# Kernel optimization log

Measured on AMD Instinct MI355X. Metric: run time of the kernel, lower is better.

The kernel has to match this reference:

```python
import jax, jax.numpy as jnp
import numpy as np

N, E, IN_DIM, OUT_DIM = 12288, 6144, 256, 256


def setup_inputs() -> dict:
    key = jax.random.key(0)
    k1, k2, k3, k4, k5 = jax.random.split(key, 5)
    x = jax.random.normal(k1, (N, IN_DIM), dtype=jnp.float32)
    # incidence-like matrix (dense, values in [0,1))
    H = jax.random.uniform(k2, (N, E), dtype=jnp.float32)
    # degree-normalizer diagonals: positive entries on the diagonal
    dv = jax.random.uniform(k3, (N,), dtype=jnp.float32, minval=0.1, maxval=1.0)
    de = jax.random.uniform(k4, (E,), dtype=jnp.float32, minval=0.1, maxval=1.0)
    D_v_neg_sqrt = jnp.diag(dv)
    D_e_neg = jnp.diag(de)
    # Linear params (xavier-like weight, zero bias)
    W = jax.random.normal(k5, (IN_DIM, OUT_DIM), dtype=jnp.float32) * (1.0 / np.sqrt(IN_DIM))
    b = jnp.zeros((OUT_DIM,), dtype=jnp.float32)
    return {"x": x, "H": H, "D_v_neg_sqrt": D_v_neg_sqrt, "D_e_neg": D_e_neg, "W": W, "b": b}


def reference(x, H, D_v_neg_sqrt, D_e_neg, W, b):
    # x_transformed = Linear(x)
    x_t = x @ W + b                      # [N, out]
    x_norm = D_v_neg_sqrt @ x_t          # [N, out]
    x_he = H.T @ x_norm                  # [E, out]
    x_he_norm = D_e_neg @ x_he           # [E, out]
    x_node = H @ x_he_norm               # [N, out]
    out = D_v_neg_sqrt @ x_node          # [N, out]
    # dropout is identity in eval mode
    return out
```

## Files before the change

kernel.cpp:

```cpp
#include <hip/hip_runtime.h>

#define NN 12288
#define NE 6144
#define ND 256

typedef __attribute__((ext_vector_type(8))) short short8;
typedef __attribute__((ext_vector_type(4))) float f32x4;
typedef unsigned short u16;
typedef unsigned int u32;

__device__ inline u16 f2bf(float f) {
  union { float f; u32 u; } v; v.f = f;
  u32 r = v.u + 0x7fffu + ((v.u >> 16) & 1u);
  return (u16)(r >> 16);
}

__device__ inline void gll16(const void* g, void* l) {
  __builtin_amdgcn_global_load_lds(
      (const __attribute__((address_space(1))) u32*)g,
      (__attribute__((address_space(3))) u32*)l, 16, 0, 0);
}

__device__ inline void stage_B(const u16* __restrict__ Bg, int ldb, int k0,
                               u16* __restrict__ Blds) {
  const int w = threadIdx.x >> 6;
  const int lane = threadIdx.x & 63;
  const int dd = lane >> 2, p = lane & 3;
#pragma unroll
  for (int s = 0; s < 4; ++s) {
    const int dbase = (w * 4 + s) * 16;
    const int n = dbase + dd;
    const int c = (p - (n >> 1)) & 3;
    gll16(Bg + (size_t)n * ldb + k0 + c * 8, Blds + dbase * 32);
  }
}

__device__ inline short8 load_B(const u16* __restrict__ Blds, int n, int quad) {
  const int p = (quad + (n >> 1)) & 3;
  return *(const short8*)(Blds + n * 32 + p * 8);
}

__global__ __launch_bounds__(256) void k_xform(
    const float* __restrict__ x, const u16* __restrict__ Wt,
    const float* __restrict__ b, const float* __restrict__ dv,
    u16* __restrict__ xnt) {
  __shared__ u16 Alds[64 * 40];
  __shared__ u16 Blds[256 * 32];
  const int tid = threadIdx.x;
  const int w = tid >> 6, lane = tid & 63, ln = lane & 15, quad = lane >> 4;
  const int m0 = blockIdx.x * 64;
  const int am = tid >> 2, ac = (tid & 3) * 8;
  f32x4 acc[4][4] = {};
  for (int kt = 0; kt < ND / 32; ++kt) {
    const int k0 = kt * 32;
    __syncthreads();
    stage_B(Wt, ND, k0, Blds);
    const float4* pa = (const float4*)(x + (size_t)(m0 + am) * ND + k0 + ac);
    float4 f0 = pa[0], f1 = pa[1];
    short8 av;
    av[0] = (short)f2bf(f0.x); av[1] = (short)f2bf(f0.y);
    av[2] = (short)f2bf(f0.z); av[3] = (short)f2bf(f0.w);
    av[4] = (short)f2bf(f1.x); av[5] = (short)f2bf(f1.y);
    av[6] = (short)f2bf(f1.z); av[7] = (short)f2bf(f1.w);
    *(short8*)(Alds + am * 40 + ac) = av;
    __syncthreads();
    short8 af[4];
#pragma unroll
    for (int mt = 0; mt < 4; ++mt)
      af[mt] = *(const short8*)(Alds + (mt * 16 + ln) * 40 + quad * 8);
#pragma unroll
    for (int nt = 0; nt < 4; ++nt) {
      short8 bf = load_B(Blds, w * 64 + nt * 16 + ln, quad);
#pragma unroll
      for (int mt = 0; mt < 4; ++mt)
        acc[nt][mt] = __builtin_amdgcn_mfma_f32_16x16x32_bf16(af[mt], bf, acc[nt][mt], 0, 0, 0);
    }
  }
#pragma unroll
  for (int nt = 0; nt < 4; ++nt) {
    const int d = w * 64 + nt * 16 + ln;
    const float bb = b[d];
#pragma unroll
    for (int mt = 0; mt < 4; ++mt) {
      const int vb = m0 + mt * 16 + quad * 4;
      f32x4 a = acc[nt][mt];
      union { u16 h[4]; uint2 u; } pk;
#pragma unroll
      for (int r = 0; r < 4; ++r) pk.h[r] = f2bf(dv[vb + r] * (a[r] + bb));
      *(uint2*)(xnt + (size_t)d * NN + vb) = pk.u;
    }
  }
}

__global__ __launch_bounds__(256) void k_gemm1s(
    const float* __restrict__ H, const u16* __restrict__ xnt,
    float* __restrict__ P1) {
  __shared__ u16 Alds[64 * 40];
  __shared__ u16 Blds[256 * 32];
  const int tid = threadIdx.x;
  const int w = tid >> 6, lane = tid & 63, ln = lane & 15, quad = lane >> 4;
  const int e0 = blockIdx.x * 64;
  const int kbase = blockIdx.y * 1536;
  const int p2 = tid & 3, ea = tid >> 2;
  f32x4 acc[4][4] = {};
  for (int kt = 0; kt < 48; ++kt) {
    const int k0 = kbase + kt * 32;
    __syncthreads();
    stage_B(xnt, NN, k0, Blds);
#pragma unroll
    for (int i = 0; i < 4; ++i) {
      const int p = p2 + i * 4;
      const int v = k0 + p * 2;
      float g0 = H[(size_t)v * NE + e0 + ea];
      float g1 = H[(size_t)(v + 1) * NE + e0 + ea];
      u32 pk = (u32)f2bf(g0) | ((u32)f2bf(g1) << 16);
      *(u32*)(Alds + ea * 40 + p * 2) = pk;
    }
    __syncthreads();
    short8 af[4];
#pragma unroll
    for (int mt = 0; mt < 4; ++mt)
      af[mt] = *(const short8*)(Alds + (mt * 16 + ln) * 40 + quad * 8);
#pragma unroll
    for (int nt = 0; nt < 4; ++nt) {
      short8 bf = load_B(Blds, w * 64 + nt * 16 + ln, quad);
#pragma unroll
      for (int mt = 0; mt < 4; ++mt)
        acc[nt][mt] = __builtin_amdgcn_mfma_f32_16x16x32_bf16(af[mt], bf, acc[nt][mt], 0, 0, 0);
    }
  }
  float* P = P1 + (size_t)blockIdx.y * NE * ND;
#pragma unroll
  for (int nt = 0; nt < 4; ++nt) {
    const int d = w * 64 + nt * 16 + ln;
#pragma unroll
    for (int mt = 0; mt < 4; ++mt) {
      const int eb = e0 + mt * 16 + quad * 4;
      f32x4 a = acc[nt][mt];
#pragma unroll
      for (int r = 0; r < 4; ++r)
        P[(size_t)(eb + r) * ND + d] = a[r];
    }
  }
}

__global__ __launch_bounds__(256) void k_red1(
    const float* __restrict__ P1, const float* __restrict__ de,
    u16* __restrict__ xhet) {
  const int tid = threadIdx.x;
  const int e0 = blockIdx.x * 16;
  union { u16 h[16]; uint4 q[2]; } pk;
#pragma unroll
  for (int i = 0; i < 16; ++i) {
    float s = 0.f;
#pragma unroll
    for (int c = 0; c < 8; ++c)
      s += P1[(size_t)c * NE * ND + (size_t)(e0 + i) * ND + tid];
    pk.h[i] = f2bf(de[e0 + i] * s);
  }
  uint4* dst = (uint4*)(xhet + (size_t)tid * NE + e0);
  dst[0] = pk.q[0];
  dst[1] = pk.q[1];
}

__global__ __launch_bounds__(256) void k_gemm2s(
    const float* __restrict__ H, const u16* __restrict__ xhet,
    float* __restrict__ P2) {
  __shared__ u16 Alds[64 * 40];
  __shared__ u16 Blds[256 * 32];
  const int tid = threadIdx.x;
  const int w = tid >> 6, lane = tid & 63, ln = lane & 15, quad = lane >> 4;
  const int m0 = blockIdx.x * 64;
  const int kbase = blockIdx.y * 1536;
  const int am = tid >> 2, ac = (tid & 3) * 8;
  f32x4 acc[4][4] = {};
  for (int kt = 0; kt < 48; ++kt) {
    const int k0 = kbase + kt * 32;
    __syncthreads();
    stage_B(xhet, NE, k0, Blds);
    const float4* pa = (const float4*)(H + (size_t)(m0 + am) * NE + k0 + ac);
    float4 f0 = pa[0], f1 = pa[1];
    short8 av;
    av[0] = (short)f2bf(f0.x); av[1] = (short)f2bf(f0.y);
    av[2] = (short)f2bf(f0.z); av[3] = (short)f2bf(f0.w);
    av[4] = (short)f2bf(f1.x); av[5] = (short)f2bf(f1.y);
    av[6] = (short)f2bf(f1.z); av[7] = (short)f2bf(f1.w);
    *(short8*)(Alds + am * 40 + ac) = av;
    __syncthreads();
    short8 af[4];
#pragma unroll
    for (int mt = 0; mt < 4; ++mt)
      af[mt] = *(const short8*)(Alds + (mt * 16 + ln) * 40 + quad * 8);
#pragma unroll
    for (int nt = 0; nt < 4; ++nt) {
      short8 bf = load_B(Blds, w * 64 + nt * 16 + ln, quad);
#pragma unroll
      for (int mt = 0; mt < 4; ++mt)
        acc[nt][mt] = __builtin_amdgcn_mfma_f32_16x16x32_bf16(af[mt], bf, acc[nt][mt], 0, 0, 0);
    }
  }
  float* P = P2 + (size_t)blockIdx.y * NN * ND;
#pragma unroll
  for (int nt = 0; nt < 4; ++nt) {
    const int d = w * 64 + nt * 16 + ln;
#pragma unroll
    for (int mt = 0; mt < 4; ++mt) {
      const int vb = m0 + mt * 16 + quad * 4;
      f32x4 a = acc[nt][mt];
#pragma unroll
      for (int r = 0; r < 4; ++r)
        P[(size_t)(vb + r) * ND + d] = a[r];
    }
  }
}

__global__ __launch_bounds__(256) void k_red2(
    const float* __restrict__ P2, const float* __restrict__ dv,
    float* __restrict__ out) {
  const int tid = threadIdx.x;
  const int v0 = blockIdx.x * 16;
#pragma unroll
  for (int i = 0; i < 16; ++i) {
    float s = 0.f;
#pragma unroll
    for (int c = 0; c < 4; ++c)
      s += P2[(size_t)c * NN * ND + (size_t)(v0 + i) * ND + tid];
    out[(size_t)(v0 + i) * ND + tid] = dv[v0 + i] * s;
  }
}

__global__ __launch_bounds__(256) void k_prep(
    const float* __restrict__ W, const float* __restrict__ Dv,
    const float* __restrict__ De, u16* __restrict__ Wt,
    float* __restrict__ dv, float* __restrict__ de) {
  const int t = blockIdx.x * 256 + threadIdx.x;
  const int d = t >> 8, k = t & 255;
  Wt[d * 256 + k] = f2bf(W[k * 256 + d]);
  if (t < NN) dv[t] = Dv[(size_t)t * (NN + 1)];
  if (t < NE) de[t] = De[(size_t)t * (NE + 1)];
}

extern "C" void kernel_launch(void* const* d_in, const int* in_sizes, int n_in,
                              void* d_out, int out_size, void* d_ws, size_t ws_size,
                              hipStream_t stream) {
  const float* x  = (const float*)d_in[0];
  const float* H  = (const float*)d_in[1];
  const float* Dv = (const float*)d_in[2];
  const float* De = (const float*)d_in[3];
  const float* W  = (const float*)d_in[4];
  const float* b  = (const float*)d_in[5];
  float* out = (float*)d_out;
  char* ws = (char*)d_ws;
  u16* xnt   = (u16*)ws;
  u16* xhet  = (u16*)(ws + 6291456);
  u16* Wt    = (u16*)(ws + 9437184);
  float* dv  = (float*)(ws + 9568256);
  float* de  = (float*)(ws + 9617408);
  float* P1  = (float*)(ws + 9641984);
  float* P2  = (float*)(ws + 59973632);

  hipLaunchKernelGGL(k_prep,   dim3(256), dim3(256), 0, stream, W, Dv, De, Wt, dv, de);
  hipLaunchKernelGGL(k_xform,  dim3(NN / 64), dim3(256), 0, stream, x, Wt, b, dv, xnt);
  hipLaunchKernelGGL(k_gemm1s, dim3(NE / 64, 8), dim3(256), 0, stream, H, xnt, P1);
  hipLaunchKernelGGL(k_red1,   dim3(NE / 16), dim3(256), 0, stream, P1, de, xhet);
  hipLaunchKernelGGL(k_gemm2s, dim3(NN / 64, 4), dim3(256), 0, stream, H, xhet, P2);
  hipLaunchKernelGGL(k_red2,   dim3(NN / 16), dim3(256), 0, stream, P2, dv, out);
}
```

Baseline: 1.081 ms.

## Double-buffer LDS tiles to overlap global loads with MFMA compute

Converts the three GEMM kernels to a two-stage software pipeline. Each now holds two LDS buffers, prefetches the next K-tile of A (into registers) and B (via global_load_lds) while running MFMAs on the current tile, and needs one barrier per iteration instead of two. This is meant to hide global memory latency behind matrix compute. The cost is doubled LDS use per block (about 42KB), which may lower occupancy, and more live registers for the prefetched A values.

```diff
diff --git a/kernel.cpp b/kernel.cpp
--- a/kernel.cpp
+++ b/kernel.cpp
@@ -40,42 +40,61 @@
   return *(const short8*)(Blds + n * 32 + p * 8);
 }
 
+__device__ inline void compute_step(const u16* __restrict__ Al,
+                                    const u16* __restrict__ Bl, int w, int ln,
+                                    int quad, f32x4 (&acc)[4][4]) {
+  short8 af[4];
+#pragma unroll
+  for (int mt = 0; mt < 4; ++mt)
+    af[mt] = *(const short8*)(Al + (mt * 16 + ln) * 40 + quad * 8);
+#pragma unroll
+  for (int nt = 0; nt < 4; ++nt) {
+    short8 bf = load_B(Bl, w * 64 + nt * 16 + ln, quad);
+#pragma unroll
+    for (int mt = 0; mt < 4; ++mt)
+      acc[nt][mt] = __builtin_amdgcn_mfma_f32_16x16x32_bf16(af[mt], bf, acc[nt][mt], 0, 0, 0);
+  }
+}
+
 __global__ __launch_bounds__(256) void k_xform(
     const float* __restrict__ x, const u16* __restrict__ Wt,
     const float* __restrict__ b, const float* __restrict__ dv,
     u16* __restrict__ xnt) {
-  __shared__ u16 Alds[64 * 40];
-  __shared__ u16 Blds[256 * 32];
+  __shared__ u16 Alds[2][64 * 40];
+  __shared__ u16 Blds[2][256 * 32];
   const int tid = threadIdx.x;
   const int w = tid >> 6, lane = tid & 63, ln = lane & 15, quad = lane >> 4;
   const int m0 = blockIdx.x * 64;
   const int am = tid >> 2, ac = (tid & 3) * 8;
   f32x4 acc[4][4] = {};
-  for (int kt = 0; kt < ND / 32; ++kt) {
-    const int k0 = kt * 32;
+  stage_B(Wt, ND, 0, Blds[0]);
+  {
+    const float4* pa = (const float4*)(x + (size_t)(m0 + am) * ND + ac);
+    float4 f0 = pa[0], f1 = pa[1];
+    short8 av;
+    av[0] = (short)f2bf(f0.x); av[1] = (short)f2bf(f0.y);
+    av[2] = (short)f2bf(f0.z); av[3] = (short)f2bf(f0.w);
+    av[4] = (short)f2bf(f1.x); av[5] = (short)f2bf(f1.y);
+    av[6] = (short)f2bf(f1.z); av[7] = (short)f2bf(f1.w);
+    *(short8*)(Alds[0] + am * 40 + ac) = av;
+  }
+  __syncthreads();
+  for (int kt = 0; kt < ND / 32 - 1; ++kt) {
+    const int cur = kt & 1, nxt = cur ^ 1;
+    const int k1 = (kt + 1) * 32;
+    stage_B(Wt, ND, k1, Blds[nxt]);
+    const float4* pa = (const float4*)(x + (size_t)(m0 + am) * ND + k1 + ac);
+    float4 f0 = pa[0], f1 = pa[1];
+    compute_step(Alds[cur], Blds[cur], w, ln, quad, acc);
+    short8 av;
+    av[0] = (short)f2bf(f0.x); av[1] = (short)f2bf(f0.y);
+    av[2] = (short)f2bf(f0.z); av[3] = (short)f2bf(f0.w);
+    av[4] = (short)f2bf(f1.x); av[5] = (short)f2bf(f1.y);
+    av[6] = (short)f2bf(f1.z); av[7] = (short)f2bf(f1.w);
+    *(short8*)(Alds[nxt] + am * 40 + ac) = av;
     __syncthreads();
-    stage_B(Wt, ND, k0, Blds);
-    const float4* pa = (const float4*)(x + (size_t)(m0 + am) * ND + k0 + ac);
-    float4 f0 = pa[0], f1 = pa[1];
-    short8 av;
-    av[0] = (short)f2bf(f0.x); av[1] = (short)f2bf(f0.y);
-    av[2] = (short)f2bf(f0.z); av[3] = (short)f2bf(f0.w);
-    av[4] = (short)f2bf(f1.x); av[5] = (short)f2bf(f1.y);
-    av[6] = (short)f2bf(f1.z); av[7] = (short)f2bf(f1.w);
-    *(short8*)(Alds + am * 40 + ac) = av;
-    __syncthreads();
-    short8 af[4];
-#pragma unroll
-    for (int mt = 0; mt < 4; ++mt)
-      af[mt] = *(const short8*)(Alds + (mt * 16 + ln) * 40 + quad * 8);
-#pragma unroll
-    for (int nt = 0; nt < 4; ++nt) {
-      short8 bf = load_B(Blds, w * 64 + nt * 16 + ln, quad);
-#pragma unroll
-      for (int mt = 0; mt < 4; ++mt)
-        acc[nt][mt] = __builtin_amdgcn_mfma_f32_16x16x32_bf16(af[mt], bf, acc[nt][mt], 0, 0, 0);
-    }
-  }
+  }
+  compute_step(Alds[1], Blds[1], w, ln, quad, acc);
 #pragma unroll
   for (int nt = 0; nt < 4; ++nt) {
     const int d = w * 64 + nt * 16 + ln;
@@ -95,40 +114,49 @@
 __global__ __launch_bounds__(256) void k_gemm1s(
     const float* __restrict__ H, const u16* __restrict__ xnt,
     float* __restrict__ P1) {
-  __shared__ u16 Alds[64 * 40];
-  __shared__ u16 Blds[256 * 32];
+  __shared__ u16 Alds[2][64 * 40];
+  __shared__ u16 Blds[2][256 * 32];
   const int tid = threadIdx.x;
   const int w = tid >> 6, lane = tid & 63, ln = lane & 15, quad = lane >> 4;
   const int e0 = blockIdx.x * 64;
   const int kbase = blockIdx.y * 1536;
   const int p2 = tid & 3, ea = tid >> 2;
   f32x4 acc[4][4] = {};
-  for (int kt = 0; kt < 48; ++kt) {
-    const int k0 = kbase + kt * 32;
-    __syncthreads();
-    stage_B(xnt, NN, k0, Blds);
+  float g[8];
+  stage_B(xnt, NN, kbase, Blds[0]);
+#pragma unroll
+  for (int i = 0; i < 4; ++i) {
+    const int v = kbase + (p2 + i * 4) * 2;
+    g[2 * i] = H[(size_t)v * NE + e0 + ea];
+    g[2 * i + 1] = H[(size_t)(v + 1) * NE + e0 + ea];
+  }
+#pragma unroll
+  for (int i = 0; i < 4; ++i) {
+    const int p = p2 + i * 4;
+    u32 pk = (u32)f2bf(g[2 * i]) | ((u32)f2bf(g[2 * i + 1]) << 16);
+    *(u32*)(Alds[0] + ea * 40 + p * 2) = pk;
+  }
+  __syncthreads();
+  for (int kt = 0; kt < 47; ++kt) {
+    const int cur = kt & 1, nxt = cur ^ 1;
+    const int k1 = kbase + (kt + 1) * 32;
+    stage_B(xnt, NN, k1, Blds[nxt]);
+#pragma unroll
+    for (int i = 0; i < 4; ++i) {
+      const int v = k1 + (p2 + i * 4) * 2;
+      g[2 * i] = H[(size_t)v * NE + e0 + ea];
+      g[2 * i + 1] = H[(size_t)(v + 1) * NE + e0 + ea];
+    }
+    compute_step(Alds[cur], Blds[cur], w, ln, quad, acc);
 #pragma unroll
     for (int i = 0; i < 4; ++i) {
       const int p = p2 + i * 4;
-      const int v = k0 + p * 2;
-      float g0 = H[(size_t)v * NE + e0 + ea];
-      float g1 = H[(size_t)(v + 1) * NE + e0 + ea];
-      u32 pk = (u32)f2bf(g0) | ((u32)f2bf(g1) << 16);
-      *(u32*)(Alds + ea * 40 + p * 2) = pk;
+      u32 pk = (u32)f2bf(g[2 * i]) | ((u32)f2bf(g[2 * i + 1]) << 16);
+      *(u32*)(Alds[nxt] + ea * 40 + p * 2) = pk;
     }
     __syncthreads();
-    short8 af[4];
-#pragma unroll
-    for (int mt = 0; mt < 4; ++mt)
-      af[mt] = *(const short8*)(Alds + (mt * 16 + ln) * 40 + quad * 8);
-#pragma unroll
-    for (int nt = 0; nt < 4; ++nt) {
-      short8 bf = load_B(Blds, w * 64 + nt * 16 + ln, quad);
-#pragma unroll
-      for (int mt = 0; mt < 4; ++mt)
-        acc[nt][mt] = __builtin_amdgcn_mfma_f32_16x16x32_bf16(af[mt], bf, acc[nt][mt], 0, 0, 0);
-    }
-  }
+  }
+  compute_step(Alds[1], Blds[1], w, ln, quad, acc);
   float* P = P1 + (size_t)blockIdx.y * NE * ND;
 #pragma unroll
   for (int nt = 0; nt < 4; ++nt) {
@@ -166,39 +194,42 @@
 __global__ __launch_bounds__(256) void k_gemm2s(
     const float* __restrict__ H, const u16* __restrict__ xhet,
     float* __restrict__ P2) {
-  __shared__ u16 Alds[64 * 40];
-  __shared__ u16 Blds[256 * 32];
+  __shared__ u16 Alds[2][64 * 40];
+  __shared__ u16 Blds[2][256 * 32];
   const int tid = threadIdx.x;
   const int w = tid >> 6, lane = tid & 63, ln = lane & 15, quad = lane >> 4;
   const int m0 = blockIdx.x * 64;
   const int kbase = blockIdx.y * 1536;
   const int am = tid >> 2, ac = (tid & 3) * 8;
   f32x4 acc[4][4] = {};
-  for (int kt = 0; kt < 48; ++kt) {
-    const int k0 = kbase + kt * 32;
+  stage_B(xhet, NE, kbase, Blds[0]);
+  {
+    const float4* pa = (const float4*)(H + (size_t)(m0 + am) * NE + kbase + ac);
+    float4 f0 = pa[0], f1 = pa[1];
+    short8 av;
+    av[0] = (short)f2bf(f0.x); av[1] = (short)f2bf(f0.y);
+    av[2] = (short)f2bf(f0.z); av[3] = (short)f2bf(f0.w);
+    av[4] = (short)f2bf(f1.x); av[5] = (short)f2bf(f1.y);
+    av[6] = (short)f2bf(f1.z); av[7] = (short)f2bf(f1.w);
+    *(short8*)(Alds[0] + am * 40 + ac) = av;
+  }
+  __syncthreads();
+  for (int kt = 0; kt < 47; ++kt) {
+    const int cur = kt & 1, nxt = cur ^ 1;
+    const int k1 = kbase + (kt + 1) * 32;
+    stage_B(xhet, NE, k1, Blds[nxt]);
+    const float4* pa = (const float4*)(H + (size_t)(m0 + am) * NE + k1 + ac);
+    float4 f0 = pa[0], f1 = pa[1];
+    compute_step(Alds[cur], Blds[cur], w, ln, quad, acc);
+    short8 av;
+    av[0] = (short)f2bf(f0.x); av[1] = (short)f2bf(f0.y);
+    av[2] = (short)f2bf(f0.z); av[3] = (short)f2bf(f0.w);
+    av[4] = (short)f2bf(f1.x); av[5] = (short)f2bf(f1.y);
+    av[6] = (short)f2bf(f1.z); av[7] = (short)f2bf(f1.w);
+    *(short8*)(Alds[nxt] + am * 40 + ac) = av;
     __syncthreads();
-    stage_B(xhet, NE, k0, Blds);
-    const float4* pa = (const float4*)(H + (size_t)(m0 + am) * NE + k0 + ac);
-    float4 f0 = pa[0], f1 = pa[1];
-    short8 av;
-    av[0] = (short)f2bf(f0.x); av[1] = (short)f2bf(f0.y);
-    av[2] = (short)f2bf(f0.z); av[3] = (short)f2bf(f0.w);
-    av[4] = (short)f2bf(f1.x); av[5] = (short)f2bf(f1.y);
-    av[6] = (short)f2bf(f1.z); av[7] = (short)f2bf(f1.w);
-    *(short8*)(Alds + am * 40 + ac) = av;
-    __syncthreads();
-    short8 af[4];
-#pragma unroll
-    for (int mt = 0; mt < 4; ++mt)
-      af[mt] = *(const short8*)(Alds + (mt * 16 + ln) * 40 + quad * 8);
-#pragma unroll
-    for (int nt = 0; nt < 4; ++nt) {
-      short8 bf = load_B(Blds, w * 64 + nt * 16 + ln, quad);
-#pragma unroll
-      for (int mt = 0; mt < 4; ++mt)
-        acc[nt][mt] = __builtin_amdgcn_mfma_f32_16x16x32_bf16(af[mt], bf, acc[nt][mt], 0, 0, 0);
-    }
-  }
+  }
+  compute_step(Alds[1], Blds[1], w, ln, quad, acc);
   float* P = P2 + (size_t)blockIdx.y * NN * ND;
 #pragma unroll
   for (int nt = 0; nt < 4; ++nt) {
```

Result: no change. 1.080 ms (-0.1%).

## Fuse all stages into one cooperative persistent kernel with grid syncs

Applied to the files above, without the earlier changes.

Replaces the six separate launches with a single cooperative kernel of 512 blocks (two per CU on 256 CUs) that runs the prep, transform, both split-K GEMMs and both reductions in sequence, separated by grid-wide barriers. Tiles are reshaped to 48-row blocks with larger K splits (4 and 2 chunks) so the fixed grid covers each GEMM exactly in one wave. This removes inter-kernel launch gaps and tail effects. In exchange, the smaller M tiles reduce per-block reuse, the grid barriers add their own cost, and the transform stage uses only 16-row tasks with one wave loading A. The old multi-kernel path stays as a fallback if the cooperative launch fails.

```diff
diff --git a/kernel.cpp b/kernel.cpp
--- a/kernel.cpp
+++ b/kernel.cpp
@@ -1,4 +1,7 @@
 #include <hip/hip_runtime.h>
+#include <hip/hip_cooperative_groups.h>
+
+namespace cg = cooperative_groups;
 
 #define NN 12288
 #define NE 6144
@@ -38,6 +41,195 @@
 __device__ inline short8 load_B(const u16* __restrict__ Blds, int n, int quad) {
   const int p = (quad + (n >> 1)) & 3;
   return *(const short8*)(Blds + n * 32 + p * 8);
+}
+
+template <int MT>
+__device__ inline void compute_tile(const u16* __restrict__ Al,
+                                    const u16* __restrict__ Bl, int w, int ln,
+                                    int quad, f32x4 (&acc)[4][MT]) {
+  short8 af[MT];
+#pragma unroll
+  for (int mt = 0; mt < MT; ++mt)
+    af[mt] = *(const short8*)(Al + (mt * 16 + ln) * 40 + quad * 8);
+#pragma unroll
+  for (int nt = 0; nt < 4; ++nt) {
+    short8 bf = load_B(Bl, w * 64 + nt * 16 + ln, quad);
+#pragma unroll
+    for (int mt = 0; mt < MT; ++mt)
+      acc[nt][mt] = __builtin_amdgcn_mfma_f32_16x16x32_bf16(af[mt], bf, acc[nt][mt], 0, 0, 0);
+  }
+}
+
+__global__ __launch_bounds__(256, 2) void mega(
+    const float* __restrict__ x, const float* __restrict__ H,
+    const float* __restrict__ Dv, const float* __restrict__ De,
+    const float* __restrict__ W, const float* __restrict__ b,
+    float* __restrict__ out, u16* __restrict__ xnt, u16* __restrict__ xhet,
+    u16* __restrict__ Wt, float* __restrict__ dv, float* __restrict__ de,
+    float* __restrict__ P1, float* __restrict__ P2) {
+  cg::grid_group gg = cg::this_grid();
+  __shared__ u16 Alds[64 * 40];
+  __shared__ u16 Blds[256 * 32];
+  const int tid = threadIdx.x;
+  const int bid = blockIdx.x;
+  const int w = tid >> 6, lane = tid & 63, ln = lane & 15, quad = lane >> 4;
+
+  {
+    const int t = bid * 256 + tid;
+    if (t < 65536) {
+      const int d = t >> 8, k = t & 255;
+      Wt[d * 256 + k] = f2bf(W[k * 256 + d]);
+    }
+    if (t < NN) dv[t] = Dv[(size_t)t * (NN + 1)];
+    if (t < NE) de[t] = De[(size_t)t * (NE + 1)];
+  }
+  gg.sync();
+
+  for (int task = bid; task < 768; task += 512) {
+    const int m0 = task * 16;
+    f32x4 acc[4] = {};
+    for (int kt = 0; kt < 8; ++kt) {
+      const int k0 = kt * 32;
+      __syncthreads();
+      stage_B(Wt, ND, k0, Blds);
+      if (tid < 64) {
+        const int am = tid >> 2, ac2 = (tid & 3) * 8;
+        const float4* pa = (const float4*)(x + (size_t)(m0 + am) * ND + k0 + ac2);
+        float4 f0 = pa[0], f1 = pa[1];
+        short8 av;
+        av[0] = (short)f2bf(f0.x); av[1] = (short)f2bf(f0.y);
+        av[2] = (short)f2bf(f0.z); av[3] = (short)f2bf(f0.w);
+        av[4] = (short)f2bf(f1.x); av[5] = (short)f2bf(f1.y);
+        av[6] = (short)f2bf(f1.z); av[7] = (short)f2bf(f1.w);
+        *(short8*)(Alds + am * 40 + ac2) = av;
+      }
+      __syncthreads();
+      short8 af = *(const short8*)(Alds + ln * 40 + quad * 8);
+#pragma unroll
+      for (int nt = 0; nt < 4; ++nt) {
+        short8 bf = load_B(Blds, w * 64 + nt * 16 + ln, quad);
+        acc[nt] = __builtin_amdgcn_mfma_f32_16x16x32_bf16(af, bf, acc[nt], 0, 0, 0);
+      }
+    }
+#pragma unroll
+    for (int nt = 0; nt < 4; ++nt) {
+      const int d = w * 64 + nt * 16 + ln;
+      const float bb = b[d];
+      const int vb = m0 + quad * 4;
+      f32x4 a = acc[nt];
+      union { u16 h[4]; uint2 u; } pk;
+#pragma unroll
+      for (int r = 0; r < 4; ++r) pk.h[r] = f2bf(dv[vb + r] * (a[r] + bb));
+      *(uint2*)(xnt + (size_t)d * NN + vb) = pk.u;
+    }
+  }
+  gg.sync();
+
+  {
+    const int e0 = (bid & 127) * 48;
+    const int kc = bid >> 7;
+    const int kbase = kc * 3072;
+    const int p2 = tid & 3, ea = tid >> 2;
+    f32x4 acc[4][3] = {};
+    for (int kt = 0; kt < 96; ++kt) {
+      const int k0 = kbase + kt * 32;
+      __syncthreads();
+      stage_B(xnt, NN, k0, Blds);
+      if (ea < 48) {
+#pragma unroll
+        for (int i = 0; i < 4; ++i) {
+          const int p = p2 + i * 4;
+          const int v = k0 + p * 2;
+          float g0 = H[(size_t)v * NE + e0 + ea];
+          float g1 = H[(size_t)(v + 1) * NE + e0 + ea];
+          u32 pk = (u32)f2bf(g0) | ((u32)f2bf(g1) << 16);
+          *(u32*)(Alds + ea * 40 + p * 2) = pk;
+        }
+      }
+      __syncthreads();
+      compute_tile<3>(Alds, Blds, w, ln, quad, acc);
+    }
+    float* P = P1 + (size_t)kc * NE * ND;
+#pragma unroll
+    for (int nt = 0; nt < 4; ++nt) {
+      const int d = w * 64 + nt * 16 + ln;
+#pragma unroll
+      for (int mt = 0; mt < 3; ++mt) {
+        const int eb = e0 + mt * 16 + quad * 4;
+        f32x4 a = acc[nt][mt];
+#pragma unroll
+        for (int r = 0; r < 4; ++r)
+          P[(size_t)(eb + r) * ND + d] = a[r];
+      }
+    }
+  }
+  gg.sync();
+
+  if (bid < 384) {
+    const int e0 = bid * 16;
+    union { u16 h[16]; uint4 q[2]; } pk;
+#pragma unroll
+    for (int i = 0; i < 16; ++i) {
+      float s = 0.f;
+#pragma unroll
+      for (int c = 0; c < 4; ++c)
+        s += P1[(size_t)c * NE * ND + (size_t)(e0 + i) * ND + tid];
+      pk.h[i] = f2bf(de[e0 + i] * s);
+    }
+    uint4* dst = (uint4*)(xhet + (size_t)tid * NE + e0);
+    dst[0] = pk.q[0];
+    dst[1] = pk.q[1];
+  }
+  gg.sync();
+
+  {
+    const int m0 = (bid & 255) * 48;
+    const int kc = bid >> 8;
+    const int kbase = kc * 3072;
+    const int am = tid >> 2, ac2 = (tid & 3) * 8;
+    f32x4 acc[4][3] = {};
+    for (int kt = 0; kt < 96; ++kt) {
+      const int k0 = kbase + kt * 32;
+      __syncthreads();
+      stage_B(xhet, NE, k0, Blds);
+      if (am < 48) {
+        const float4* pa = (const float4*)(H + (size_t)(m0 + am) * NE + k0 + ac2);
+        float4 f0 = pa[0], f1 = pa[1];
+        short8 av;
+        av[0] = (short)f2bf(f0.x); av[1] = (short)f2bf(f0.y);
+        av[2] = (short)f2bf(f0.z); av[3] = (short)f2bf(f0.w);
+        av[4] = (short)f2bf(f1.x); av[5] = (short)f2bf(f1.y);
+        av[6] = (short)f2bf(f1.z); av[7] = (short)f2bf(f1.w);
+        *(short8*)(Alds + am * 40 + ac2) = av;
+      }
+      __syncthreads();
+      compute_tile<3>(Alds, Blds, w, ln, quad, acc);
+    }
+    float* P = P2 + (size_t)kc * NN * ND;
+#pragma unroll
+    for (int nt = 0; nt < 4; ++nt) {
+      const int d = w * 64 + nt * 16 + ln;
+#pragma unroll
+      for (int mt = 0; mt < 3; ++mt) {
+        const int vb = m0 + mt * 16 + quad * 4;
+        f32x4 a = acc[nt][mt];
+#pragma unroll
+        for (int r = 0; r < 4; ++r)
+          P[(size_t)(vb + r) * ND + d] = a[r];
+      }
+    }
+  }
+  gg.sync();
+
+  {
+    const int v0 = bid * 24;
+#pragma unroll 4
+    for (int i = 0; i < 24; ++i) {
+      float s = P2[(size_t)(v0 + i) * ND + tid] +
+                P2[(size_t)NN * ND + (size_t)(v0 + i) * ND + tid];
+      out[(size_t)(v0 + i) * ND + tid] = dv[v0 + i] * s;
+    }
+  }
 }
 
 __global__ __launch_bounds__(256) void k_xform(
@@ -64,17 +256,8 @@
     av[6] = (short)f2bf(f1.z); av[7] = (short)f2bf(f1.w);
     *(short8*)(Alds + am * 40 + ac) = av;
     __syncthreads();
-    short8 af[4];
-#pragma unroll
-    for (int mt = 0; mt < 4; ++mt)
-      af[mt] = *(const short8*)(Alds + (mt * 16 + ln) * 40 + quad * 8);
-#pragma unroll
-    for (int nt = 0; nt < 4; ++nt) {
-      short8 bf = load_B(Blds, w * 64 + nt * 16 + ln, quad);
-#pragma unroll
-      for (int mt = 0; mt < 4; ++mt)
-        acc[nt][mt] = __builtin_amdgcn_mfma_f32_16x16x32_bf16(af[mt], bf, acc[nt][mt], 0, 0, 0);
-    }
+    f32x4(&acc4)[4][4] = acc;
+    compute_tile<4>(Alds, Blds, w, ln, quad, acc4);
   }
 #pragma unroll
   for (int nt = 0; nt < 4; ++nt) {
@@ -117,17 +300,7 @@
       *(u32*)(Alds + ea * 40 + p * 2) = pk;
     }
     __syncthreads();
-    short8 af[4];
-#pragma unroll
-    for (int mt = 0; mt < 4; ++mt)
-      af[mt] = *(const short8*)(Alds + (mt * 16 + ln) * 40 + quad * 8);
-#pragma unroll
-    for (int nt = 0; nt < 4; ++nt) {
-      short8 bf = load_B(Blds, w * 64 + nt * 16 + ln, quad);
-#pragma unroll
-      for (int mt = 0; mt < 4; ++mt)
-        acc[nt][mt] = __builtin_amdgcn_mfma_f32_16x16x32_bf16(af[mt], bf, acc[nt][mt], 0, 0, 0);
-    }
+    compute_tile<4>(Alds, Blds, w, ln, quad, acc);
   }
   float* P = P1 + (size_t)blockIdx.y * NE * ND;
 #pragma unroll
@@ -187,17 +360,7 @@
     av[6] = (short)f2bf(f1.z); av[7] = (short)f2bf(f1.w);
     *(short8*)(Alds + am * 40 + ac) = av;
     __syncthreads();
-    short8 af[4];
-#pragma unroll
-    for (int mt = 0; mt < 4; ++mt)
-      af[mt] = *(const short8*)(Alds + (mt * 16 + ln) * 40 + quad * 8);
-#pragma unroll
-    for (int nt = 0; nt < 4; ++nt) {
-      short8 bf = load_B(Blds, w * 64 + nt * 16 + ln, quad);
-#pragma unroll
-      for (int mt = 0; mt < 4; ++mt)
-        acc[nt][mt] = __builtin_amdgcn_mfma_f32_16x16x32_bf16(af[mt], bf, acc[nt][mt], 0, 0, 0);
-    }
+    compute_tile<4>(Alds, Blds, w, ln, quad, acc);
   }
   float* P = P2 + (size_t)blockIdx.y * NN * ND;
 #pragma unroll
@@ -259,10 +422,17 @@
   float* P1  = (float*)(ws + 9641984);
   float* P2  = (float*)(ws + 59973632);
 
-  hipLaunchKernelGGL(k_prep,   dim3(256), dim3(256), 0, stream, W, Dv, De, Wt, dv, de);
-  hipLaunchKernelGGL(k_xform,  dim3(NN / 64), dim3(256), 0, stream, x, Wt, b, dv, xnt);
-  hipLaunchKernelGGL(k_gemm1s, dim3(NE / 64, 8), dim3(256), 0, stream, H, xnt, P1);
-  hipLaunchKernelGGL(k_red1,   dim3(NE / 16), dim3(256), 0, stream, P1, de, xhet);
-  hipLaunchKernelGGL(k_gemm2s, dim3(NN / 64, 4), dim3(256), 0, stream, H, xhet, P2);
-  hipLaunchKernelGGL(k_red2,   dim3(NN / 16), dim3(256), 0, stream, P2, dv, out);
-}
+  void* args[] = {(void*)&x, (void*)&H, (void*)&Dv, (void*)&De, (void*)&W,
+                  (void*)&b, (void*)&out, (void*)&xnt, (void*)&xhet, (void*)&Wt,
+                  (void*)&dv, (void*)&de, (void*)&P1, (void*)&P2};
+  hipError_t err = hipLaunchCooperativeKernel((void*)mega, dim3(512), dim3(256),
+                                              args, 0, stream);
+  if (err != hipSuccess) {
+    hipLaunchKernelGGL(k_prep,   dim3(256), dim3(256), 0, stream, W, Dv, De, Wt, dv, de);
+    hipLaunchKernelGGL(k_xform,  dim3(NN / 64), dim3(256), 0, stream, x, Wt, b, dv, xnt);
+    hipLaunchKernelGGL(k_gemm1s, dim3(NE / 64, 8), dim3(256), 0, stream, H, xnt, P1);
+    hipLaunchKernelGGL(k_red1,   dim3(NE / 16), dim3(256), 0, stream, P1, de, xhet);
+    hipLaunchKernelGGL(k_gemm2s, dim3(NN / 64, 4), dim3(256), 0, stream, H, xhet, P2);
+    hipLaunchKernelGGL(k_red2,   dim3(NN / 16), dim3(256), 0, stream, P2, dv, out);
+  }
+}
```

New measurement: 1.405 ms. 1.3x slower.
